# Optimization experiments

Hardware: AMD Instinct MI355X
Metric: run time of the kernel (lower is better)

The kernel has to match this reference:

```python
import jax, jax.numpy as jnp
import numpy as np

N_NODES = 50000


def _gine(x, src, dst, edge_embed, lin_w, lin_b, nn_w, nn_b):
    # PyG GINEConv (eps=0): out = nn(x + sum_{j->i} ReLU(x_j + lin(edge_attr)))
    e = edge_embed @ lin_w + lin_b              # [E, d_in]
    msg = jax.nn.relu(x[src] + e)               # gather + fuse, [E, d_in]
    agg = jax.ops.segment_sum(msg, dst, num_segments=N_NODES)  # scatter-add, [N, d_in]
    return (x + agg) @ nn_w + nn_b              # small MLP, [N, d_out]


def setup_inputs() -> dict:
    key = jax.random.key(0)
    ks = jax.random.split(key, 20)
    E = 800000
    h = 128
    sc = lambda f_in: 1.0 / np.sqrt(f_in)
    inp = {
        "x": jax.random.normal(ks[0], (N_NODES, 1), jnp.float32),
        "edge_index": jax.random.randint(ks[1], (2, E), 0, N_NODES, jnp.int64),
        "edge_attr": jax.random.normal(ks[2], (E, 1), jnp.float32),
        "em_w": jax.random.normal(ks[3], (1, h), jnp.float32) * sc(1),
        "em_b": jnp.zeros((h,), jnp.float32),
        "l1_w": jax.random.normal(ks[4], (h, 1), jnp.float32) * sc(h),
        "l1_b": jnp.zeros((1,), jnp.float32),
        "n1_w": jax.random.normal(ks[5], (1, h), jnp.float32) * sc(1),
        "n1_b": jnp.zeros((h,), jnp.float32),
        "l2_w": jax.random.normal(ks[6], (h, h), jnp.float32) * sc(h),
        "l2_b": jnp.zeros((h,), jnp.float32),
        "n2_w": jax.random.normal(ks[7], (h, h), jnp.float32) * sc(h),
        "n2_b": jnp.zeros((h,), jnp.float32),
        "l3_w": jax.random.normal(ks[8], (h, h), jnp.float32) * sc(h),
        "l3_b": jnp.zeros((h,), jnp.float32),
        "n3_w": jax.random.normal(ks[9], (h, h), jnp.float32) * sc(h),
        "n3_b": jnp.zeros((h,), jnp.float32),
        "dec_w": jax.random.normal(ks[10], (2 * h, 1), jnp.float32) * sc(2 * h),
        "dec_b": jnp.zeros((1,), jnp.float32),
    }
    return inp


def reference(x, edge_index, edge_attr, em_w, em_b, l1_w, l1_b, n1_w, n1_b,
              l2_w, l2_b, n2_w, n2_b, l3_w, l3_b, n3_w, n3_b, dec_w, dec_b):
    src, dst = edge_index[0], edge_index[1]
    edge_embed = edge_attr @ em_w + em_b                      # [E, 128]
    hdn = _gine(x,   src, dst, edge_embed, l1_w, l1_b, n1_w, n1_b)
    hdn = _gine(hdn, src, dst, edge_embed, l2_w, l2_b, n2_w, n2_b)
    hdn = _gine(hdn, src, dst, edge_embed, l3_w, l3_b, n3_w, n3_b)
    h_cat = jnp.concatenate([hdn[src], hdn[dst]], axis=-1)    # [E, 256]
    return h_cat @ dec_w + dec_b                              # [E, 1]
```

## Files before the change

kernel.cpp:

```cpp
#include <hip/hip_runtime.h>

#define H 128
#define CAPC 3072


typedef unsigned long long ull;
using bf16x8 = __attribute__((ext_vector_type(8))) short;
using f32x4  = __attribute__((ext_vector_type(4))) float;

__device__ __forceinline__ float bf2f(unsigned short v) {
  return __uint_as_float(((unsigned)v) << 16);
}
__device__ __forceinline__ unsigned short bf16r(float v) {
  unsigned u = __float_as_uint(v);
  u = (u + 0x7FFFu + ((u >> 16) & 1u)) >> 16;
  return (unsigned short)u;
}
__device__ __forceinline__ unsigned bf16pair(float a, float b) {
  return (unsigned)bf16r(a) | ((unsigned)bf16r(b) << 16);
}
__device__ __forceinline__ int rfl(int v) {
  return __builtin_amdgcn_readfirstlane(v);
}

__global__ __launch_bounds__(256) void init_consts(
    const float* __restrict__ em_w, const float* __restrict__ em_b,
    const float* __restrict__ l1_w, const float* __restrict__ l1_b,
    const float* __restrict__ l2_w, const float* __restrict__ l2_b,
    const float* __restrict__ n1_b,
    const float* __restrict__ l3_w, const float* __restrict__ l3_b,
    const float* __restrict__ n2w, const float* __restrict__ n3w,
    const float* __restrict__ n3b, const float* __restrict__ dec_w,
    float* __restrict__ consts, int* __restrict__ cursor,
    unsigned short* __restrict__ w2t) {
  if (blockIdx.x > 0) {
    const int i = (blockIdx.x - 1) * 256 + threadIdx.x;
    if (i < H * H) {
      const int j = i >> 7, k = i & (H - 1);
      w2t[k * H + j] = bf16r(n2w[i]);
    }
    return;
  }
  const int k = threadIdx.x;
  cursor[k] = 0;
  cursor[k + 256] = 0;
  __shared__ float sa[H], sc[H];
  if (k < H) {
    float u2 = 0.f, c2 = 0.f, u3 = 0.f, c3 = 0.f, vA = 0.f, vB = 0.f;
    for (int j = 0; j < H; ++j) {
      const float ew = em_w[j], eb = em_b[j];
      u2 = fmaf(ew, l2_w[j * H + k], u2);
      c2 = fmaf(eb, l2_w[j * H + k], c2);
      u3 = fmaf(ew, l3_w[j * H + k], u3);
      c3 = fmaf(eb, l3_w[j * H + k], c3);
      vA = fmaf(n3w[k * H + j], dec_w[j], vA);
      vB = fmaf(n3w[k * H + j], dec_w[H + j], vB);
    }
    consts[2 + k]         = u2;
    consts[2 + H + k]     = c2 + l2_b[k] + n1_b[k];
    consts[2 + 2 * H + k] = u3;
    consts[2 + 3 * H + k] = c3 + l3_b[k];
    consts[514 + k]       = vA;
    consts[642 + k]       = vB;
    sa[k] = em_w[k] * l1_w[k];
    sc[k] = em_b[k] * l1_w[k];
  }
  __syncthreads();
  for (int s = 64; s > 0; s >>= 1) {
    if (k < s) { sa[k] += sa[k + s]; sc[k] += sc[k + s]; }
    __syncthreads();
  }
  if (k == 0) { consts[0] = sa[0]; consts[1] = sc[0] + l1_b[0]; }
  __syncthreads();
  if (k < H) {
    sa[k] = n3b[k] * dec_w[k];
    sc[k] = n3b[k] * dec_w[H + k];
  }
  __syncthreads();
  for (int s = 64; s > 0; s >>= 1) {
    if (k < s) { sa[k] += sa[k + s]; sc[k] += sc[k + s]; }
    __syncthreads();
  }
  if (k == 0) { consts[770] = sa[0]; consts[771] = sc[0]; }
}

__global__ __launch_bounds__(1024) void bin_scatter(
    const int* __restrict__ src, const int* __restrict__ dst,
    const float* __restrict__ ea, int* __restrict__ cursor,
    ull* __restrict__ spc, int E, int NBUCK) {
  __shared__ int lhist[512];
  __shared__ int lbase[512];
  const int tid = threadIdx.x;
  const int base = blockIdx.x * 2048 + tid * 2;
  if (tid < 512) lhist[tid] = 0;
  __syncthreads();
  int s_[2], d_[2], b_[2], r_[2];
  float a_[2];
#pragma unroll
  for (int j = 0; j < 2; ++j) {
    const int e = base + j;
    if (e < E) {
      s_[j] = src[e]; d_[j] = dst[e]; a_[j] = ea[e];
      b_[j] = d_[j] >> 7;
      r_[j] = atomicAdd(&lhist[b_[j]], 1);
    } else {
      b_[j] = -1;
    }
  }
  __syncthreads();
  if (tid < NBUCK && lhist[tid] > 0)
    lbase[tid] = atomicAdd(&cursor[tid], lhist[tid]);
  __syncthreads();
#pragma unroll
  for (int j = 0; j < 2; ++j) {
    if (b_[j] >= 0) {
      const int pl = lbase[b_[j]] + r_[j];
      if (pl < CAPC)
        spc[(size_t)b_[j] * CAPC + pl] =
            ((ull)(unsigned)(s_[j] | ((d_[j] & 127) << 16)) << 32) |
            (ull)(unsigned)__float_as_uint(a_[j]);
    }
  }
}

__global__ __launch_bounds__(1024) void fine_scatter(
    const int* __restrict__ cursor, const ull* __restrict__ spc,
    const float* __restrict__ x, const float* __restrict__ consts,
    int2* __restrict__ spf, int* __restrict__ rowstart,
    float* __restrict__ s1, int N) {
  __shared__ int lh[128];
  __shared__ int sd[128];
  __shared__ int cur[128];
  __shared__ int2 pay[CAPC];
  const int tid = threadIdx.x;
  const int b = blockIdx.x;
  const int cnt = min(cursor[b], CAPC);
  const size_t rbase = (size_t)b * CAPC;
  if (tid < 128) lh[tid] = 0;
  __syncthreads();
  for (int i = tid; i < cnt; i += 1024)
    atomicAdd(&lh[(int)((spc[rbase + i] >> 48) & 127u)], 1);
  __syncthreads();
  if (tid < 128) sd[tid] = lh[tid];
  __syncthreads();
  for (int off = 1; off < 128; off <<= 1) {
    int t = 0;
    if (tid < 128 && tid >= off) t = sd[tid - off];
    __syncthreads();
    if (tid < 128) sd[tid] += t;
    __syncthreads();
  }
  if (tid < 128) {
    const int ex = sd[tid] - lh[tid];
    cur[tid] = ex;
    rowstart[b * 129 + tid] = (int)rbase + ex;
    if (tid == 0) rowstart[b * 129 + 128] = (int)rbase + cnt;
  }
  __syncthreads();
  for (int i = tid; i < cnt; i += 1024) {
    const ull payv = spc[rbase + i];
    const int dl = (int)((payv >> 48) & 127u);
    const int pos = atomicAdd(&cur[dl], 1);
    pay[pos] = make_int2((int)((payv >> 32) & 0xFFFFu), (int)(unsigned)payv);
  }
  __syncthreads();
  for (int i = tid; i < cnt; i += 1024) spf[rbase + i] = pay[i];
  const int lane = tid & 63, w = tid >> 6;
  const float a1 = consts[0], c1 = consts[1];
  for (int i = w; i < 128; i += 16) {
    const int n = (b << 7) + i;
    if (n >= N) break;
    const int rsl = sd[i] - lh[i], ci = lh[i];
    float part = 0.f;
    for (int j = lane; j < ci; j += 64) {
      const int2 pv = pay[rsl + j];
      part += fmaxf(x[pv.x] + fmaf(a1, __int_as_float(pv.y), c1), 0.f);
    }
#pragma unroll
    for (int o = 32; o >= 1; o >>= 1) part += __shfl_xor(part, o, 64);
    if (lane == 0) s1[n] = x[n] + part;
  }
}

__global__ __launch_bounds__(1024) void layer2_fused(
    const int* __restrict__ rowstart, const int2* __restrict__ sp,
    const float* __restrict__ s1, const float* __restrict__ n1w,
    const float* __restrict__ n1b, const float* __restrict__ consts,
    const unsigned short* __restrict__ w2t, const float* __restrict__ n2b,
    unsigned short* __restrict__ h2b, int N) {
  __shared__ unsigned short t2s[16][136];
  __shared__ unsigned short hs[16][128];
  const int tid = threadIdx.x, w = tid >> 6, lane = tid & 63;
  const int node0 = blockIdx.x * 16;
  {
    const int n = rfl(node0 + w);
    if (n < N) {
      const int rb = (n >> 7) * 129 + (n & 127);
      const int rs = rfl(rowstart[rb]), re = rfl(rowstart[rb + 1]);
      const float w0 = n1w[lane],            w1 = n1w[lane + 64];
      const float u0 = consts[2 + lane],     u1 = consts[2 + lane + 64];
      const float c0 = consts[2 + H + lane], c1 = consts[2 + H + lane + 64];
      float acc0 = 0.f, acc1 = 0.f;
      int j = rs;
      for (; j + 4 <= re; j += 4) {
        int sx[4];
        float av[4], sv[4];
#pragma unroll
        for (int u = 0; u < 4; ++u) {
          const int2 ev = sp[j + u];
          sx[u] = rfl(ev.x);
          av[u] = __int_as_float(rfl(ev.y));
        }
#pragma unroll
        for (int u = 0; u < 4; ++u) sv[u] = s1[sx[u]];
#pragma unroll
        for (int u = 0; u < 4; ++u) {
          acc0 += fmaxf(fmaf(sv[u], w0, fmaf(av[u], u0, c0)), 0.f);
          acc1 += fmaxf(fmaf(sv[u], w1, fmaf(av[u], u1, c1)), 0.f);
        }
      }
      for (; j < re; ++j) {
        const int2 ev = sp[j];
        const int sx = rfl(ev.x);
        const float av = __int_as_float(rfl(ev.y));
        const float sv = s1[sx];
        acc0 += fmaxf(fmaf(sv, w0, fmaf(av, u0, c0)), 0.f);
        acc1 += fmaxf(fmaf(sv, w1, fmaf(av, u1, c1)), 0.f);
      }
      const float sn = s1[n];
      t2s[w][lane]      = bf16r(fmaf(sn, w0, n1b[lane])      + acc0);
      t2s[w][lane + 64] = bf16r(fmaf(sn, w1, n1b[lane + 64]) + acc1);
    } else {
      t2s[w][lane] = 0;
      t2s[w][lane + 64] = 0;
    }
  }
  __syncthreads();
  if (w < 8) {
    const int t = w, col = lane & 15, quad = lane >> 4;
    const bf16x8 a0 = *(const bf16x8*)&t2s[col][quad * 8];
    const bf16x8 a1 = *(const bf16x8*)&t2s[col][32 + quad * 8];
    const bf16x8 a2 = *(const bf16x8*)&t2s[col][64 + quad * 8];
    const bf16x8 a3 = *(const bf16x8*)&t2s[col][96 + quad * 8];
    const bf16x8* bcol =
        (const bf16x8*)(w2t + (size_t)(t * 16 + col) * H + quad * 8);
    f32x4 acc = {0.f, 0.f, 0.f, 0.f};
    acc = __builtin_amdgcn_mfma_f32_16x16x32_bf16(a0, bcol[0], acc, 0, 0, 0);
    acc = __builtin_amdgcn_mfma_f32_16x16x32_bf16(a1, bcol[4], acc, 0, 0, 0);
    acc = __builtin_amdgcn_mfma_f32_16x16x32_bf16(a2, bcol[8], acc, 0, 0, 0);
    acc = __builtin_amdgcn_mfma_f32_16x16x32_bf16(a3, bcol[12], acc, 0, 0, 0);
    const float bias = n2b[t * 16 + col];
#pragma unroll
    for (int r = 0; r < 4; ++r)
      hs[quad * 4 + r][t * 16 + col] = bf16r(acc[r] + bias);
  }
  __syncthreads();
  const int row = tid >> 6, word = tid & 63;
  ((unsigned*)h2b)[(size_t)(node0 + row) * 64 + word] =
      ((const unsigned*)hs)[row * 64 + word];
}

__global__ __launch_bounds__(256) void layer3_dot(
    const int* __restrict__ rowstart, const int2* __restrict__ sp,
    const unsigned short* __restrict__ h2b, const float* __restrict__ consts,
    float* __restrict__ p, float* __restrict__ q, int N) {
  const int n = rfl((blockIdx.x * blockDim.x + threadIdx.x) >> 6);
  const int lane = threadIdx.x & 63;
  if (n >= N) return;
  const int k0 = 2 * lane;
  const float u0 = consts[2 + 2 * H + k0], u1 = consts[2 + 2 * H + k0 + 1];
  const float c0 = consts[2 + 3 * H + k0], c1 = consts[2 + 3 * H + k0 + 1];
  const float vA0 = consts[514 + k0], vA1 = consts[514 + k0 + 1];
  const float vB0 = consts[642 + k0], vB1 = consts[642 + k0 + 1];
  const int rb = (n >> 7) * 129 + (n & 127);
  const int rs = rfl(rowstart[rb]), re = rfl(rowstart[rb + 1]);
  float acc0 = 0.f, acc1 = 0.f;
  int j = rs;
  for (; j + 8 <= re; j += 8) {
    int ss[8];
    float aa[8];
    ushort2 hh[8];
#pragma unroll
    for (int u = 0; u < 8; ++u) {
      const int2 ev = sp[j + u];
      ss[u] = rfl(ev.x);
      aa[u] = __int_as_float(rfl(ev.y));
    }
#pragma unroll
    for (int u = 0; u < 8; ++u)
      hh[u] = *(const ushort2*)&h2b[(size_t)ss[u] * H + k0];
#pragma unroll
    for (int u = 0; u < 8; ++u) {
      acc0 += fmaxf(bf2f(hh[u].x) + fmaf(aa[u], u0, c0), 0.f);
      acc1 += fmaxf(bf2f(hh[u].y) + fmaf(aa[u], u1, c1), 0.f);
    }
  }
  for (; j + 4 <= re; j += 4) {
    int ss[4];
    float aa[4];
    ushort2 hh[4];
#pragma unroll
    for (int u = 0; u < 4; ++u) {
      const int2 ev = sp[j + u];
      ss[u] = rfl(ev.x);
      aa[u] = __int_as_float(rfl(ev.y));
    }
#pragma unroll
    for (int u = 0; u < 4; ++u)
      hh[u] = *(const ushort2*)&h2b[(size_t)ss[u] * H + k0];
#pragma unroll
    for (int u = 0; u < 4; ++u) {
      acc0 += fmaxf(bf2f(hh[u].x) + fmaf(aa[u], u0, c0), 0.f);
      acc1 += fmaxf(bf2f(hh[u].y) + fmaf(aa[u], u1, c1), 0.f);
    }
  }
  for (; j < re; ++j) {
    const int2 ev = sp[j];
    const int s0 = rfl(ev.x);
    const float a0 = __int_as_float(rfl(ev.y));
    const ushort2 hv = *(const ushort2*)&h2b[(size_t)s0 * H + k0];
    acc0 += fmaxf(bf2f(hv.x) + fmaf(a0, u0, c0), 0.f);
    acc1 += fmaxf(bf2f(hv.y) + fmaf(a0, u1, c1), 0.f);
  }
  const ushort2 hn = *(const ushort2*)&h2b[(size_t)n * H + k0];
  const float t0 = bf2f(hn.x) + acc0;
  const float t1 = bf2f(hn.y) + acc1;
  float pd = t0 * vA0 + t1 * vA1;
  float qd = t0 * vB0 + t1 * vB1;
#pragma unroll
  for (int o = 32; o >= 1; o >>= 1) {
    pd += __shfl_xor(pd, o, 64);
    qd += __shfl_xor(qd, o, 64);
  }
  if (lane == 0) {
    p[n] = pd + consts[770];
    q[n] = qd + consts[771];
  }
}

__global__ void final_kernel(const int* __restrict__ src,
                             const int* __restrict__ dst,
                             const float* __restrict__ p,
                             const float* __restrict__ q,
                             const float* __restrict__ dec_b,
                             float* __restrict__ out, int E) {
  const int e0 = (blockIdx.x * blockDim.x + threadIdx.x) * 2;
  if (e0 + 1 < E) {
    const int2 s2 = *(const int2*)&src[e0];
    const int2 d2 = *(const int2*)&dst[e0];
    const float db = dec_b[0];
    float2 o;
    o.x = p[s2.x] + q[d2.x] + db;
    o.y = p[s2.y] + q[d2.y] + db;
    *(float2*)&out[e0] = o;
  } else if (e0 < E) {
    out[e0] = p[src[e0]] + q[dst[e0]] + dec_b[0];
  }
}

extern "C" void kernel_launch(void* const* d_in, const int* in_sizes, int n_in,
                              void* d_out, int out_size, void* d_ws, size_t ws_size,
                              hipStream_t stream) {
  const float* x     = (const float*)d_in[0];
  const int*   ei    = (const int*)d_in[1];
  const float* ea    = (const float*)d_in[2];
  const float* em_w  = (const float*)d_in[3];
  const float* em_b  = (const float*)d_in[4];
  const float* l1_w  = (const float*)d_in[5];
  const float* l1_b  = (const float*)d_in[6];
  const float* n1_w  = (const float*)d_in[7];
  const float* n1_b  = (const float*)d_in[8];
  const float* l2_w  = (const float*)d_in[9];
  const float* l2_b  = (const float*)d_in[10];
  const float* n2_w  = (const float*)d_in[11];
  const float* n2_b  = (const float*)d_in[12];
  const float* l3_w  = (const float*)d_in[13];
  const float* l3_b  = (const float*)d_in[14];
  const float* n3_w  = (const float*)d_in[15];
  const float* n3_b  = (const float*)d_in[16];
  const float* dec_w = (const float*)d_in[17];
  const float* dec_b = (const float*)d_in[18];
  float* out = (float*)d_out;

  const int N = in_sizes[0];
  const int E = in_sizes[2];
  const int* src = ei;
  const int* dst = ei + E;

  const int NBUCK  = (N + 127) >> 7;
  const int NBATCH = (E + 2047) >> 11;
  const int NPAD   = ((N + 15) / 16) * 16;
  const int NT16   = NPAD / 16;

  float* ws       = (float*)d_ws;
  float* consts   = ws;
  ull*   spc      = (ull*)(ws + 1024);
  int2*  spf      = (int2*)(spc + (size_t)NBUCK * CAPC);
  unsigned short* h2b = (unsigned short*)(spf + (size_t)NBUCK * CAPC);
  unsigned short* w2t = h2b + (size_t)NPAD * H;
  float* s1       = (float*)(w2t + H * H);
  float* p        = s1 + N;
  float* q        = p + N;
  int*   cursor   = (int*)(q + N);
  int*   rowstart = cursor + 512;

  init_consts<<<65, 256, 0, stream>>>(em_w, em_b, l1_w, l1_b, l2_w, l2_b,
                                      n1_b, l3_w, l3_b, n2_w, n3_w, n3_b,
                                      dec_w, consts, cursor, w2t);
  bin_scatter<<<NBATCH, 1024, 0, stream>>>(src, dst, ea, cursor, spc, E, NBUCK);
  fine_scatter<<<NBUCK, 1024, 0, stream>>>(cursor, spc, x, consts, spf,
                                           rowstart, s1, N);
  layer2_fused<<<NT16, 1024, 0, stream>>>(rowstart, spf, s1, n1_w, n1_b,
                                          consts, w2t, n2_b, h2b, N);
  layer3_dot<<<(N + 3) / 4, 256, 0, stream>>>(rowstart, spf, h2b, consts,
                                              p, q, N);
  final_kernel<<<(E / 2 + 255) / 256, 256, 0, stream>>>(src, dst, p, q, dec_b,
                                                        out, E);
}
```

Before: 213.6 us.

## Merge all stages into one cooperative persistent kernel with grid syncs

Replaces six separate kernel launches with one cooperative kernel of 256 blocks of 1024 threads. The blocks loop over the work of each stage and separate stages with grid.sync(). Shared memory is reused across stages through a union. The goal is to remove launch overhead and the gaps between kernels. In exchange it caps concurrency at 256 resident blocks, so the gather-heavy layer loops lose the occupancy they had with many smaller launches. Grid-wide barriers also cost time.

```diff
diff --git a/kernel.cpp b/kernel.cpp
--- a/kernel.cpp
+++ b/kernel.cpp
@@ -1,4 +1,7 @@
 #include <hip/hip_runtime.h>
+#include <hip/hip_cooperative_groups.h>
+
+namespace cg = cooperative_groups;
 
 #define H 128
 #define CAPC 3072
@@ -16,345 +19,349 @@
   u = (u + 0x7FFFu + ((u >> 16) & 1u)) >> 16;
   return (unsigned short)u;
 }
-__device__ __forceinline__ unsigned bf16pair(float a, float b) {
-  return (unsigned)bf16r(a) | ((unsigned)bf16r(b) << 16);
-}
 __device__ __forceinline__ int rfl(int v) {
   return __builtin_amdgcn_readfirstlane(v);
 }
 
-__global__ __launch_bounds__(256) void init_consts(
+__global__ __launch_bounds__(1024) void mega(
+    const float* __restrict__ x, const int* __restrict__ src,
+    const int* __restrict__ dst, const float* __restrict__ ea,
     const float* __restrict__ em_w, const float* __restrict__ em_b,
     const float* __restrict__ l1_w, const float* __restrict__ l1_b,
+    const float* __restrict__ n1w, const float* __restrict__ n1b,
     const float* __restrict__ l2_w, const float* __restrict__ l2_b,
-    const float* __restrict__ n1_b,
+    const float* __restrict__ n2w, const float* __restrict__ n2b,
     const float* __restrict__ l3_w, const float* __restrict__ l3_b,
-    const float* __restrict__ n2w, const float* __restrict__ n3w,
-    const float* __restrict__ n3b, const float* __restrict__ dec_w,
+    const float* __restrict__ n3w, const float* __restrict__ n3b,
+    const float* __restrict__ dec_w, const float* __restrict__ dec_b,
     float* __restrict__ consts, int* __restrict__ cursor,
-    unsigned short* __restrict__ w2t) {
-  if (blockIdx.x > 0) {
-    const int i = (blockIdx.x - 1) * 256 + threadIdx.x;
-    if (i < H * H) {
-      const int j = i >> 7, k = i & (H - 1);
-      w2t[k * H + j] = bf16r(n2w[i]);
-    }
-    return;
-  }
-  const int k = threadIdx.x;
-  cursor[k] = 0;
-  cursor[k + 256] = 0;
-  __shared__ float sa[H], sc[H];
-  if (k < H) {
-    float u2 = 0.f, c2 = 0.f, u3 = 0.f, c3 = 0.f, vA = 0.f, vB = 0.f;
-    for (int j = 0; j < H; ++j) {
-      const float ew = em_w[j], eb = em_b[j];
-      u2 = fmaf(ew, l2_w[j * H + k], u2);
-      c2 = fmaf(eb, l2_w[j * H + k], c2);
-      u3 = fmaf(ew, l3_w[j * H + k], u3);
-      c3 = fmaf(eb, l3_w[j * H + k], c3);
-      vA = fmaf(n3w[k * H + j], dec_w[j], vA);
-      vB = fmaf(n3w[k * H + j], dec_w[H + j], vB);
-    }
-    consts[2 + k]         = u2;
-    consts[2 + H + k]     = c2 + l2_b[k] + n1_b[k];
-    consts[2 + 2 * H + k] = u3;
-    consts[2 + 3 * H + k] = c3 + l3_b[k];
-    consts[514 + k]       = vA;
-    consts[642 + k]       = vB;
-    sa[k] = em_w[k] * l1_w[k];
-    sc[k] = em_b[k] * l1_w[k];
-  }
-  __syncthreads();
-  for (int s = 64; s > 0; s >>= 1) {
-    if (k < s) { sa[k] += sa[k + s]; sc[k] += sc[k + s]; }
-    __syncthreads();
-  }
-  if (k == 0) { consts[0] = sa[0]; consts[1] = sc[0] + l1_b[0]; }
-  __syncthreads();
-  if (k < H) {
-    sa[k] = n3b[k] * dec_w[k];
-    sc[k] = n3b[k] * dec_w[H + k];
-  }
-  __syncthreads();
-  for (int s = 64; s > 0; s >>= 1) {
-    if (k < s) { sa[k] += sa[k + s]; sc[k] += sc[k + s]; }
-    __syncthreads();
-  }
-  if (k == 0) { consts[770] = sa[0]; consts[771] = sc[0]; }
-}
-
-__global__ __launch_bounds__(1024) void bin_scatter(
-    const int* __restrict__ src, const int* __restrict__ dst,
-    const float* __restrict__ ea, int* __restrict__ cursor,
-    ull* __restrict__ spc, int E, int NBUCK) {
-  __shared__ int lhist[512];
-  __shared__ int lbase[512];
+    unsigned short* __restrict__ w2t, ull* __restrict__ spc,
+    int2* __restrict__ spf, int* __restrict__ rowstart,
+    float* __restrict__ s1, unsigned short* __restrict__ h2b,
+    float* __restrict__ p, float* __restrict__ q, float* __restrict__ out,
+    int N, int E, int NBUCK, int NBATCH, int NT16) {
+  cg::grid_group grid = cg::this_grid();
   const int tid = threadIdx.x;
-  const int base = blockIdx.x * 2048 + tid * 2;
-  if (tid < 512) lhist[tid] = 0;
-  __syncthreads();
-  int s_[2], d_[2], b_[2], r_[2];
-  float a_[2];
-#pragma unroll
-  for (int j = 0; j < 2; ++j) {
-    const int e = base + j;
-    if (e < E) {
-      s_[j] = src[e]; d_[j] = dst[e]; a_[j] = ea[e];
-      b_[j] = d_[j] >> 7;
-      r_[j] = atomicAdd(&lhist[b_[j]], 1);
-    } else {
-      b_[j] = -1;
-    }
-  }
-  __syncthreads();
-  if (tid < NBUCK && lhist[tid] > 0)
-    lbase[tid] = atomicAdd(&cursor[tid], lhist[tid]);
-  __syncthreads();
-#pragma unroll
-  for (int j = 0; j < 2; ++j) {
-    if (b_[j] >= 0) {
-      const int pl = lbase[b_[j]] + r_[j];
-      if (pl < CAPC)
-        spc[(size_t)b_[j] * CAPC + pl] =
-            ((ull)(unsigned)(s_[j] | ((d_[j] & 127) << 16)) << 32) |
-            (ull)(unsigned)__float_as_uint(a_[j]);
-    }
-  }
-}
-
-__global__ __launch_bounds__(1024) void fine_scatter(
-    const int* __restrict__ cursor, const ull* __restrict__ spc,
-    const float* __restrict__ x, const float* __restrict__ consts,
-    int2* __restrict__ spf, int* __restrict__ rowstart,
-    float* __restrict__ s1, int N) {
-  __shared__ int lh[128];
-  __shared__ int sd[128];
-  __shared__ int cur[128];
-  __shared__ int2 pay[CAPC];
-  const int tid = threadIdx.x;
-  const int b = blockIdx.x;
-  const int cnt = min(cursor[b], CAPC);
-  const size_t rbase = (size_t)b * CAPC;
-  if (tid < 128) lh[tid] = 0;
-  __syncthreads();
-  for (int i = tid; i < cnt; i += 1024)
-    atomicAdd(&lh[(int)((spc[rbase + i] >> 48) & 127u)], 1);
-  __syncthreads();
-  if (tid < 128) sd[tid] = lh[tid];
-  __syncthreads();
-  for (int off = 1; off < 128; off <<= 1) {
-    int t = 0;
-    if (tid < 128 && tid >= off) t = sd[tid - off];
-    __syncthreads();
-    if (tid < 128) sd[tid] += t;
-    __syncthreads();
-  }
-  if (tid < 128) {
-    const int ex = sd[tid] - lh[tid];
-    cur[tid] = ex;
-    rowstart[b * 129 + tid] = (int)rbase + ex;
-    if (tid == 0) rowstart[b * 129 + 128] = (int)rbase + cnt;
-  }
-  __syncthreads();
-  for (int i = tid; i < cnt; i += 1024) {
-    const ull payv = spc[rbase + i];
-    const int dl = (int)((payv >> 48) & 127u);
-    const int pos = atomicAdd(&cur[dl], 1);
-    pay[pos] = make_int2((int)((payv >> 32) & 0xFFFFu), (int)(unsigned)payv);
-  }
-  __syncthreads();
-  for (int i = tid; i < cnt; i += 1024) spf[rbase + i] = pay[i];
-  const int lane = tid & 63, w = tid >> 6;
-  const float a1 = consts[0], c1 = consts[1];
-  for (int i = w; i < 128; i += 16) {
-    const int n = (b << 7) + i;
-    if (n >= N) break;
-    const int rsl = sd[i] - lh[i], ci = lh[i];
-    float part = 0.f;
-    for (int j = lane; j < ci; j += 64) {
-      const int2 pv = pay[rsl + j];
-      part += fmaxf(x[pv.x] + fmaf(a1, __int_as_float(pv.y), c1), 0.f);
-    }
-#pragma unroll
-    for (int o = 32; o >= 1; o >>= 1) part += __shfl_xor(part, o, 64);
-    if (lane == 0) s1[n] = x[n] + part;
-  }
-}
-
-__global__ __launch_bounds__(1024) void layer2_fused(
-    const int* __restrict__ rowstart, const int2* __restrict__ sp,
-    const float* __restrict__ s1, const float* __restrict__ n1w,
-    const float* __restrict__ n1b, const float* __restrict__ consts,
-    const unsigned short* __restrict__ w2t, const float* __restrict__ n2b,
-    unsigned short* __restrict__ h2b, int N) {
-  __shared__ unsigned short t2s[16][136];
-  __shared__ unsigned short hs[16][128];
-  const int tid = threadIdx.x, w = tid >> 6, lane = tid & 63;
-  const int node0 = blockIdx.x * 16;
-  {
-    const int n = rfl(node0 + w);
+  const int bid = blockIdx.x;
+  const int GRID = gridDim.x;
+
+  __shared__ union {
+    struct { int lhist[512]; int lbase[512]; } bp;
+    struct { int lh[128]; int sd[128]; int cur[128]; int2 pay[CAPC]; } fp;
+    struct { unsigned short t2s[16][136]; unsigned short hs[16][128]; } l2;
+  } u;
+  __shared__ float sred[2][H];
+
+  if (bid == 0) {
+    const int k = tid;
+    if (k < H) {
+      float u2 = 0.f, c2 = 0.f;
+      for (int j = 0; j < H; ++j) {
+        u2 = fmaf(em_w[j], l2_w[j * H + k], u2);
+        c2 = fmaf(em_b[j], l2_w[j * H + k], c2);
+      }
+      consts[2 + k]     = u2;
+      consts[2 + H + k] = c2 + l2_b[k] + n1b[k];
+      sred[0][k] = em_w[k] * l1_w[k];
+      sred[1][k] = em_b[k] * l1_w[k];
+    }
+    __syncthreads();
+    for (int s = 64; s > 0; s >>= 1) {
+      if (k < s) { sred[0][k] += sred[0][k + s]; sred[1][k] += sred[1][k + s]; }
+      __syncthreads();
+    }
+    if (k == 0) { consts[0] = sred[0][0]; consts[1] = sred[1][0] + l1_b[0]; }
+  } else if (bid <= 16) {
+    const int i = (bid - 1) * 1024 + tid;
+    const int j = i >> 7, k = i & (H - 1);
+    w2t[k * H + j] = bf16r(n2w[i]);
+  } else if (bid == 17) {
+    if (tid < 512) cursor[tid] = 0;
+    const int k = tid;
+    if (k < H) {
+      sred[0][k] = n3b[k] * dec_w[k];
+      sred[1][k] = n3b[k] * dec_w[H + k];
+    }
+    __syncthreads();
+    for (int s = 64; s > 0; s >>= 1) {
+      if (k < s) { sred[0][k] += sred[0][k + s]; sred[1][k] += sred[1][k + s]; }
+      __syncthreads();
+    }
+    if (k == 0) { consts[770] = sred[0][0]; consts[771] = sred[1][0]; }
+  } else if (bid == 18) {
+    const int k = tid;
+    if (k < H) {
+      float u3 = 0.f, c3 = 0.f;
+      for (int j = 0; j < H; ++j) {
+        u3 = fmaf(em_w[j], l3_w[j * H + k], u3);
+        c3 = fmaf(em_b[j], l3_w[j * H + k], c3);
+      }
+      consts[2 + 2 * H + k] = u3;
+      consts[2 + 3 * H + k] = c3 + l3_b[k];
+    }
+  } else if (bid == 19) {
+    const int k = tid;
+    if (k < H) {
+      float vA = 0.f, vB = 0.f;
+      for (int j = 0; j < H; ++j) {
+        vA = fmaf(n3w[k * H + j], dec_w[j], vA);
+        vB = fmaf(n3w[k * H + j], dec_w[H + j], vB);
+      }
+      consts[514 + k] = vA;
+      consts[642 + k] = vB;
+    }
+  }
+  grid.sync();
+
+  for (int ch = bid; ch < NBATCH; ch += GRID) {
+    __syncthreads();
+    if (tid < 512) u.bp.lhist[tid] = 0;
+    __syncthreads();
+    const int base = ch * 2048 + tid * 2;
+    int s_[2], d_[2], b_[2], r_[2];
+    float a_[2];
+#pragma unroll
+    for (int j = 0; j < 2; ++j) {
+      const int e = base + j;
+      if (e < E) {
+        s_[j] = src[e]; d_[j] = dst[e]; a_[j] = ea[e];
+        b_[j] = d_[j] >> 7;
+        r_[j] = atomicAdd(&u.bp.lhist[b_[j]], 1);
+      } else {
+        b_[j] = -1;
+      }
+    }
+    __syncthreads();
+    if (tid < NBUCK && u.bp.lhist[tid] > 0)
+      u.bp.lbase[tid] = atomicAdd(&cursor[tid], u.bp.lhist[tid]);
+    __syncthreads();
+#pragma unroll
+    for (int j = 0; j < 2; ++j) {
+      if (b_[j] >= 0) {
+        const int pl = u.bp.lbase[b_[j]] + r_[j];
+        if (pl < CAPC)
+          spc[(size_t)b_[j] * CAPC + pl] =
+              ((ull)(unsigned)(s_[j] | ((d_[j] & 127) << 16)) << 32) |
+              (ull)(unsigned)__float_as_uint(a_[j]);
+      }
+    }
+  }
+  grid.sync();
+
+  for (int b = bid; b < NBUCK; b += GRID) {
+    __syncthreads();
+    const int cnt = min(cursor[b], CAPC);
+    const size_t rbase = (size_t)b * CAPC;
+    if (tid < 128) u.fp.lh[tid] = 0;
+    __syncthreads();
+    for (int i = tid; i < cnt; i += 1024)
+      atomicAdd(&u.fp.lh[(int)((spc[rbase + i] >> 48) & 127u)], 1);
+    __syncthreads();
+    if (tid < 128) u.fp.sd[tid] = u.fp.lh[tid];
+    __syncthreads();
+    for (int off = 1; off < 128; off <<= 1) {
+      int t = 0;
+      if (tid < 128 && tid >= off) t = u.fp.sd[tid - off];
+      __syncthreads();
+      if (tid < 128) u.fp.sd[tid] += t;
+      __syncthreads();
+    }
+    if (tid < 128) {
+      const int ex = u.fp.sd[tid] - u.fp.lh[tid];
+      u.fp.cur[tid] = ex;
+      rowstart[b * 129 + tid] = (int)rbase + ex;
+      if (tid == 0) rowstart[b * 129 + 128] = (int)rbase + cnt;
+    }
+    __syncthreads();
+    for (int i = tid; i < cnt; i += 1024) {
+      const ull payv = spc[rbase + i];
+      const int dl = (int)((payv >> 48) & 127u);
+      const int pos = atomicAdd(&u.fp.cur[dl], 1);
+      u.fp.pay[pos] = make_int2((int)((payv >> 32) & 0xFFFFu), (int)(unsigned)payv);
+    }
+    __syncthreads();
+    for (int i = tid; i < cnt; i += 1024) spf[rbase + i] = u.fp.pay[i];
+    const int lane = tid & 63, w = tid >> 6;
+    const float a1 = consts[0], c1 = consts[1];
+    for (int i = w; i < 128; i += 16) {
+      const int n = (b << 7) + i;
+      if (n >= N) break;
+      const int rsl = u.fp.sd[i] - u.fp.lh[i], ci = u.fp.lh[i];
+      float part = 0.f;
+      for (int j = lane; j < ci; j += 64) {
+        const int2 pv = u.fp.pay[rsl + j];
+        part += fmaxf(x[pv.x] + fmaf(a1, __int_as_float(pv.y), c1), 0.f);
+      }
+#pragma unroll
+      for (int o = 32; o >= 1; o >>= 1) part += __shfl_xor(part, o, 64);
+      if (lane == 0) s1[n] = x[n] + part;
+    }
+  }
+  grid.sync();
+
+  for (int t = bid; t < NT16; t += GRID) {
+    __syncthreads();
+    const int node0 = t * 16;
+    const int w = tid >> 6, lane = tid & 63;
+    {
+      const int n = rfl(node0 + w);
+      if (n < N) {
+        const int rb = (n >> 7) * 129 + (n & 127);
+        const int rs = rfl(rowstart[rb]), re = rfl(rowstart[rb + 1]);
+        const float w0 = n1w[lane],            w1 = n1w[lane + 64];
+        const float u0 = consts[2 + lane],     u1 = consts[2 + lane + 64];
+        const float c0 = consts[2 + H + lane], c1 = consts[2 + H + lane + 64];
+        float acc0 = 0.f, acc1 = 0.f;
+        int j = rs;
+        for (; j + 4 <= re; j += 4) {
+          int sx[4];
+          float av[4], sv[4];
+#pragma unroll
+          for (int uu = 0; uu < 4; ++uu) {
+            const int2 ev = spf[j + uu];
+            sx[uu] = rfl(ev.x);
+            av[uu] = __int_as_float(rfl(ev.y));
+          }
+#pragma unroll
+          for (int uu = 0; uu < 4; ++uu) sv[uu] = s1[sx[uu]];
+#pragma unroll
+          for (int uu = 0; uu < 4; ++uu) {
+            acc0 += fmaxf(fmaf(sv[uu], w0, fmaf(av[uu], u0, c0)), 0.f);
+            acc1 += fmaxf(fmaf(sv[uu], w1, fmaf(av[uu], u1, c1)), 0.f);
+          }
+        }
+        for (; j < re; ++j) {
+          const int2 ev = spf[j];
+          const int sx = rfl(ev.x);
+          const float av = __int_as_float(rfl(ev.y));
+          const float sv = s1[sx];
+          acc0 += fmaxf(fmaf(sv, w0, fmaf(av, u0, c0)), 0.f);
+          acc1 += fmaxf(fmaf(sv, w1, fmaf(av, u1, c1)), 0.f);
+        }
+        const float sn = s1[n];
+        u.l2.t2s[w][lane]      = bf16r(fmaf(sn, w0, n1b[lane])      + acc0);
+        u.l2.t2s[w][lane + 64] = bf16r(fmaf(sn, w1, n1b[lane + 64]) + acc1);
+      } else {
+        u.l2.t2s[w][lane] = 0;
+        u.l2.t2s[w][lane + 64] = 0;
+      }
+    }
+    __syncthreads();
+    if (w < 8) {
+      const int tt = w, col = lane & 15, quad = lane >> 4;
+      const bf16x8 a0 = *(const bf16x8*)&u.l2.t2s[col][quad * 8];
+      const bf16x8 a1 = *(const bf16x8*)&u.l2.t2s[col][32 + quad * 8];
+      const bf16x8 a2 = *(const bf16x8*)&u.l2.t2s[col][64 + quad * 8];
+      const bf16x8 a3 = *(const bf16x8*)&u.l2.t2s[col][96 + quad * 8];
+      const bf16x8* bcol =
+          (const bf16x8*)(w2t + (size_t)(tt * 16 + col) * H + quad * 8);
+      f32x4 acc = {0.f, 0.f, 0.f, 0.f};
+      acc = __builtin_amdgcn_mfma_f32_16x16x32_bf16(a0, bcol[0], acc, 0, 0, 0);
+      acc = __builtin_amdgcn_mfma_f32_16x16x32_bf16(a1, bcol[4], acc, 0, 0, 0);
+      acc = __builtin_amdgcn_mfma_f32_16x16x32_bf16(a2, bcol[8], acc, 0, 0, 0);
+      acc = __builtin_amdgcn_mfma_f32_16x16x32_bf16(a3, bcol[12], acc, 0, 0, 0);
+      const float bias = n2b[tt * 16 + col];
+#pragma unroll
+      for (int r = 0; r < 4; ++r)
+        u.l2.hs[quad * 4 + r][tt * 16 + col] = bf16r(acc[r] + bias);
+    }
+    __syncthreads();
+    const int row = tid >> 6, word = tid & 63;
+    ((unsigned*)h2b)[(size_t)(node0 + row) * 64 + word] =
+        ((const unsigned*)u.l2.hs)[row * 64 + word];
+  }
+  grid.sync();
+
+  for (int t = bid; t < NT16; t += GRID) {
+    const int n = rfl(t * 16 + (tid >> 6));
+    const int lane = tid & 63;
     if (n < N) {
+      const int k0 = 2 * lane;
+      const float u0 = consts[2 + 2 * H + k0], u1 = consts[2 + 2 * H + k0 + 1];
+      const float c0 = consts[2 + 3 * H + k0], c1 = consts[2 + 3 * H + k0 + 1];
+      const float vA0 = consts[514 + k0], vA1 = consts[514 + k0 + 1];
+      const float vB0 = consts[642 + k0], vB1 = consts[642 + k0 + 1];
       const int rb = (n >> 7) * 129 + (n & 127);
       const int rs = rfl(rowstart[rb]), re = rfl(rowstart[rb + 1]);
-      const float w0 = n1w[lane],            w1 = n1w[lane + 64];
-      const float u0 = consts[2 + lane],     u1 = consts[2 + lane + 64];
-      const float c0 = consts[2 + H + lane], c1 = consts[2 + H + lane + 64];
       float acc0 = 0.f, acc1 = 0.f;
       int j = rs;
+      for (; j + 8 <= re; j += 8) {
+        int ss[8];
+        float aa[8];
+        ushort2 hh[8];
+#pragma unroll
+        for (int uu = 0; uu < 8; ++uu) {
+          const int2 ev = spf[j + uu];
+          ss[uu] = rfl(ev.x);
+          aa[uu] = __int_as_float(rfl(ev.y));
+        }
+#pragma unroll
+        for (int uu = 0; uu < 8; ++uu)
+          hh[uu] = *(const ushort2*)&h2b[(size_t)ss[uu] * H + k0];
+#pragma unroll
+        for (int uu = 0; uu < 8; ++uu) {
+          acc0 += fmaxf(bf2f(hh[uu].x) + fmaf(aa[uu], u0, c0), 0.f);
+          acc1 += fmaxf(bf2f(hh[uu].y) + fmaf(aa[uu], u1, c1), 0.f);
+        }
+      }
       for (; j + 4 <= re; j += 4) {
-        int sx[4];
-        float av[4], sv[4];
-#pragma unroll
-        for (int u = 0; u < 4; ++u) {
-          const int2 ev = sp[j + u];
-          sx[u] = rfl(ev.x);
-          av[u] = __int_as_float(rfl(ev.y));
-        }
-#pragma unroll
-        for (int u = 0; u < 4; ++u) sv[u] = s1[sx[u]];
-#pragma unroll
-        for (int u = 0; u < 4; ++u) {
-          acc0 += fmaxf(fmaf(sv[u], w0, fmaf(av[u], u0, c0)), 0.f);
-          acc1 += fmaxf(fmaf(sv[u], w1, fmaf(av[u], u1, c1)), 0.f);
+        int ss[4];
+        float aa[4];
+        ushort2 hh[4];
+#pragma unroll
+        for (int uu = 0; uu < 4; ++uu) {
+          const int2 ev = spf[j + uu];
+          ss[uu] = rfl(ev.x);
+          aa[uu] = __int_as_float(rfl(ev.y));
+        }
+#pragma unroll
+        for (int uu = 0; uu < 4; ++uu)
+          hh[uu] = *(const ushort2*)&h2b[(size_t)ss[uu] * H + k0];
+#pragma unroll
+        for (int uu = 0; uu < 4; ++uu) {
+          acc0 += fmaxf(bf2f(hh[uu].x) + fmaf(aa[uu], u0, c0), 0.f);
+          acc1 += fmaxf(bf2f(hh[uu].y) + fmaf(aa[uu], u1, c1), 0.f);
         }
       }
       for (; j < re; ++j) {
-        const int2 ev = sp[j];
-        const int sx = rfl(ev.x);
-        const float av = __int_as_float(rfl(ev.y));
-        const float sv = s1[sx];
-        acc0 += fmaxf(fmaf(sv, w0, fmaf(av, u0, c0)), 0.f);
-        acc1 += fmaxf(fmaf(sv, w1, fmaf(av, u1, c1)), 0.f);
-      }
-      const float sn = s1[n];
-      t2s[w][lane]      = bf16r(fmaf(sn, w0, n1b[lane])      + acc0);
-      t2s[w][lane + 64] = bf16r(fmaf(sn, w1, n1b[lane + 64]) + acc1);
+        const int2 ev = spf[j];
+        const int s0 = rfl(ev.x);
+        const float a0 = __int_as_float(rfl(ev.y));
+        const ushort2 hv = *(const ushort2*)&h2b[(size_t)s0 * H + k0];
+        acc0 += fmaxf(bf2f(hv.x) + fmaf(a0, u0, c0), 0.f);
+        acc1 += fmaxf(bf2f(hv.y) + fmaf(a0, u1, c1), 0.f);
+      }
+      const ushort2 hn = *(const ushort2*)&h2b[(size_t)n * H + k0];
+      const float t0 = bf2f(hn.x) + acc0;
+      const float t1 = bf2f(hn.y) + acc1;
+      float pd = t0 * vA0 + t1 * vA1;
+      float qd = t0 * vB0 + t1 * vB1;
+#pragma unroll
+      for (int o = 32; o >= 1; o >>= 1) {
+        pd += __shfl_xor(pd, o, 64);
+        qd += __shfl_xor(qd, o, 64);
+      }
+      if (lane == 0) {
+        p[n] = pd + consts[770];
+        q[n] = qd + consts[771];
+      }
+    }
+  }
+  grid.sync();
+
+  for (int i = bid * 1024 + tid; i * 2 < E; i += GRID * 1024) {
+    const int e0 = i * 2;
+    if (e0 + 1 < E) {
+      const int2 s2 = *(const int2*)&src[e0];
+      const int2 d2 = *(const int2*)&dst[e0];
+      const float db = dec_b[0];
+      float2 o;
+      o.x = p[s2.x] + q[d2.x] + db;
+      o.y = p[s2.y] + q[d2.y] + db;
+      *(float2*)&out[e0] = o;
     } else {
-      t2s[w][lane] = 0;
-      t2s[w][lane + 64] = 0;
-    }
-  }
-  __syncthreads();
-  if (w < 8) {
-    const int t = w, col = lane & 15, quad = lane >> 4;
-    const bf16x8 a0 = *(const bf16x8*)&t2s[col][quad * 8];
-    const bf16x8 a1 = *(const bf16x8*)&t2s[col][32 + quad * 8];
-    const bf16x8 a2 = *(const bf16x8*)&t2s[col][64 + quad * 8];
-    const bf16x8 a3 = *(const bf16x8*)&t2s[col][96 + quad * 8];
-    const bf16x8* bcol =
-        (const bf16x8*)(w2t + (size_t)(t * 16 + col) * H + quad * 8);
-    f32x4 acc = {0.f, 0.f, 0.f, 0.f};
-    acc = __builtin_amdgcn_mfma_f32_16x16x32_bf16(a0, bcol[0], acc, 0, 0, 0);
-    acc = __builtin_amdgcn_mfma_f32_16x16x32_bf16(a1, bcol[4], acc, 0, 0, 0);
-    acc = __builtin_amdgcn_mfma_f32_16x16x32_bf16(a2, bcol[8], acc, 0, 0, 0);
-    acc = __builtin_amdgcn_mfma_f32_16x16x32_bf16(a3, bcol[12], acc, 0, 0, 0);
-    const float bias = n2b[t * 16 + col];
-#pragma unroll
-    for (int r = 0; r < 4; ++r)
-      hs[quad * 4 + r][t * 16 + col] = bf16r(acc[r] + bias);
-  }
-  __syncthreads();
-  const int row = tid >> 6, word = tid & 63;
-  ((unsigned*)h2b)[(size_t)(node0 + row) * 64 + word] =
-      ((const unsigned*)hs)[row * 64 + word];
-}
-
-__global__ __launch_bounds__(256) void layer3_dot(
-    const int* __restrict__ rowstart, const int2* __restrict__ sp,
-    const unsigned short* __restrict__ h2b, const float* __restrict__ consts,
-    float* __restrict__ p, float* __restrict__ q, int N) {
-  const int n = rfl((blockIdx.x * blockDim.x + threadIdx.x) >> 6);
-  const int lane = threadIdx.x & 63;
-  if (n >= N) return;
-  const int k0 = 2 * lane;
-  const float u0 = consts[2 + 2 * H + k0], u1 = consts[2 + 2 * H + k0 + 1];
-  const float c0 = consts[2 + 3 * H + k0], c1 = consts[2 + 3 * H + k0 + 1];
-  const float vA0 = consts[514 + k0], vA1 = consts[514 + k0 + 1];
-  const float vB0 = consts[642 + k0], vB1 = consts[642 + k0 + 1];
-  const int rb = (n >> 7) * 129 + (n & 127);
-  const int rs = rfl(rowstart[rb]), re = rfl(rowstart[rb + 1]);
-  float acc0 = 0.f, acc1 = 0.f;
-  int j = rs;
-  for (; j + 8 <= re; j += 8) {
-    int ss[8];
-    float aa[8];
-    ushort2 hh[8];
-#pragma unroll
-    for (int u = 0; u < 8; ++u) {
-      const int2 ev = sp[j + u];
-      ss[u] = rfl(ev.x);
-      aa[u] = __int_as_float(rfl(ev.y));
-    }
-#pragma unroll
-    for (int u = 0; u < 8; ++u)
-      hh[u] = *(const ushort2*)&h2b[(size_t)ss[u] * H + k0];
-#pragma unroll
-    for (int u = 0; u < 8; ++u) {
-      acc0 += fmaxf(bf2f(hh[u].x) + fmaf(aa[u], u0, c0), 0.f);
-      acc1 += fmaxf(bf2f(hh[u].y) + fmaf(aa[u], u1, c1), 0.f);
-    }
-  }
-  for (; j + 4 <= re; j += 4) {
-    int ss[4];
-    float aa[4];
-    ushort2 hh[4];
-#pragma unroll
-    for (int u = 0; u < 4; ++u) {
-      const int2 ev = sp[j + u];
-      ss[u] = rfl(ev.x);
-      aa[u] = __int_as_float(rfl(ev.y));
-    }
-#pragma unroll
-    for (int u = 0; u < 4; ++u)
-      hh[u] = *(const ushort2*)&h2b[(size_t)ss[u] * H + k0];
-#pragma unroll
-    for (int u = 0; u < 4; ++u) {
-      acc0 += fmaxf(bf2f(hh[u].x) + fmaf(aa[u], u0, c0), 0.f);
-      acc1 += fmaxf(bf2f(hh[u].y) + fmaf(aa[u], u1, c1), 0.f);
-    }
-  }
-  for (; j < re; ++j) {
-    const int2 ev = sp[j];
-    const int s0 = rfl(ev.x);
-    const float a0 = __int_as_float(rfl(ev.y));
-    const ushort2 hv = *(const ushort2*)&h2b[(size_t)s0 * H + k0];
-    acc0 += fmaxf(bf2f(hv.x) + fmaf(a0, u0, c0), 0.f);
-    acc1 += fmaxf(bf2f(hv.y) + fmaf(a0, u1, c1), 0.f);
-  }
-  const ushort2 hn = *(const ushort2*)&h2b[(size_t)n * H + k0];
-  const float t0 = bf2f(hn.x) + acc0;
-  const float t1 = bf2f(hn.y) + acc1;
-  float pd = t0 * vA0 + t1 * vA1;
-  float qd = t0 * vB0 + t1 * vB1;
-#pragma unroll
-  for (int o = 32; o >= 1; o >>= 1) {
-    pd += __shfl_xor(pd, o, 64);
-    qd += __shfl_xor(qd, o, 64);
-  }
-  if (lane == 0) {
-    p[n] = pd + consts[770];
-    q[n] = qd + consts[771];
-  }
-}
-
-__global__ void final_kernel(const int* __restrict__ src,
-                             const int* __restrict__ dst,
-                             const float* __restrict__ p,
-                             const float* __restrict__ q,
-                             const float* __restrict__ dec_b,
-                             float* __restrict__ out, int E) {
-  const int e0 = (blockIdx.x * blockDim.x + threadIdx.x) * 2;
-  if (e0 + 1 < E) {
-    const int2 s2 = *(const int2*)&src[e0];
-    const int2 d2 = *(const int2*)&dst[e0];
-    const float db = dec_b[0];
-    float2 o;
-    o.x = p[s2.x] + q[d2.x] + db;
-    o.y = p[s2.y] + q[d2.y] + db;
-    *(float2*)&out[e0] = o;
-  } else if (e0 < E) {
-    out[e0] = p[src[e0]] + q[dst[e0]] + dec_b[0];
+      out[e0] = p[src[e0]] + q[dst[e0]] + dec_b[0];
+    }
   }
 }
 
@@ -382,15 +389,15 @@
   const float* dec_b = (const float*)d_in[18];
   float* out = (float*)d_out;
 
-  const int N = in_sizes[0];
-  const int E = in_sizes[2];
+  int N = in_sizes[0];
+  int E = in_sizes[2];
   const int* src = ei;
   const int* dst = ei + E;
 
-  const int NBUCK  = (N + 127) >> 7;
-  const int NBATCH = (E + 2047) >> 11;
-  const int NPAD   = ((N + 15) / 16) * 16;
-  const int NT16   = NPAD / 16;
+  int NBUCK  = (N + 127) >> 7;
+  int NBATCH = (E + 2047) >> 11;
+  const int NPAD = ((N + 15) / 16) * 16;
+  int NT16   = NPAD / 16;
 
   float* ws       = (float*)d_ws;
   float* consts   = ws;
@@ -404,16 +411,17 @@
   int*   cursor   = (int*)(q + N);
   int*   rowstart = cursor + 512;
 
-  init_consts<<<65, 256, 0, stream>>>(em_w, em_b, l1_w, l1_b, l2_w, l2_b,
-                                      n1_b, l3_w, l3_b, n2_w, n3_w, n3_b,
-                                      dec_w, consts, cursor, w2t);
-  bin_scatter<<<NBATCH, 1024, 0, stream>>>(src, dst, ea, cursor, spc, E, NBUCK);
-  fine_scatter<<<NBUCK, 1024, 0, stream>>>(cursor, spc, x, consts, spf,
-                                           rowstart, s1, N);
-  layer2_fused<<<NT16, 1024, 0, stream>>>(rowstart, spf, s1, n1_w, n1_b,
-                                          consts, w2t, n2_b, h2b, N);
-  layer3_dot<<<(N + 3) / 4, 256, 0, stream>>>(rowstart, spf, h2b, consts,
-                                              p, q, N);
-  final_kernel<<<(E / 2 + 255) / 256, 256, 0, stream>>>(src, dst, p, q, dec_b,
-                                                        out, E);
+  void* args[] = {
+      (void*)&x, (void*)&src, (void*)&dst, (void*)&ea,
+      (void*)&em_w, (void*)&em_b, (void*)&l1_w, (void*)&l1_b,
+      (void*)&n1_w, (void*)&n1_b, (void*)&l2_w, (void*)&l2_b,
+      (void*)&n2_w, (void*)&n2_b, (void*)&l3_w, (void*)&l3_b,
+      (void*)&n3_w, (void*)&n3_b, (void*)&dec_w, (void*)&dec_b,
+      (void*)&consts, (void*)&cursor, (void*)&w2t, (void*)&spc,
+      (void*)&spf, (void*)&rowstart, (void*)&s1, (void*)&h2b,
+      (void*)&p, (void*)&q, (void*)&out,
+      (void*)&N, (void*)&E, (void*)&NBUCK, (void*)&NBATCH, (void*)&NT16};
+
+  hipLaunchCooperativeKernel((const void*)mega, dim3(256), dim3(1024), args,
+                             0, stream);
 }
```

After: 426.6 us. 99.7% more time.
